# Kernel tuning notes

Hardware: AMD Instinct MI355X
Metric: run time of the kernel (lower is better)

Reference implementation:

```python
import jax, jax.numpy as jnp
import numpy as np

N0, N1, N2, N3 = 100000, 25000, 6250, 1600
DEG = 16
D_IN, D_H = 512, 256


def setup_inputs() -> dict:
    key = jax.random.key(0)
    ks = jax.random.split(key, 20)
    inp = {}
    inp["x"] = jax.random.normal(ks[0], (N0, D_IN), dtype=jnp.float32)
    # bipartite blocks: (src_ids into previous frontier, dst_ids into next frontier)
    inp["src0"] = jax.random.randint(ks[1], (N1 * DEG,), 0, N0)
    inp["dst0"] = jax.random.randint(ks[2], (N1 * DEG,), 0, N1)
    inp["src1"] = jax.random.randint(ks[3], (N2 * DEG,), 0, N1)
    inp["dst1"] = jax.random.randint(ks[4], (N2 * DEG,), 0, N2)
    inp["src2"] = jax.random.randint(ks[5], (N3 * DEG,), 0, N2)
    inp["dst2"] = jax.random.randint(ks[6], (N3 * DEG,), 0, N3)
    def xavier(k, shp):
        fan_in, fan_out = shp
        lim = jnp.sqrt(6.0 / (fan_in + fan_out))
        return jax.random.uniform(k, shp, jnp.float32, -lim, lim)
    inp["Ws0"] = xavier(ks[7], (D_IN, D_H)); inp["Wn0"] = xavier(ks[8], (D_IN, D_H)); inp["b0"] = jnp.zeros((D_H,), jnp.float32)
    inp["Ws1"] = xavier(ks[9], (D_H, D_H)); inp["Wn1"] = xavier(ks[10], (D_H, D_H)); inp["b1"] = jnp.zeros((D_H,), jnp.float32)
    inp["Ws2"] = xavier(ks[11], (D_H, D_H)); inp["Wn2"] = xavier(ks[12], (D_H, D_H)); inp["b2"] = jnp.zeros((D_H,), jnp.float32)
    inp["W_fc"] = xavier(ks[13], (D_H, D_H)); inp["b_fc"] = jnp.zeros((D_H,), jnp.float32)
    return inp


def _sage_mean(h, src, dst, n_dst, Ws, Wn, b):
    # DGL SAGEConv('mean') on a bipartite block: out = h_dst@Ws + mean_neigh@Wn + b
    h_dst = h[:n_dst]                                   # [n_dst, d]
    msg = h[src]                                        # [E, d] gather
    agg = jax.ops.segment_sum(msg, dst, num_segments=n_dst)
    deg = jax.ops.segment_sum(jnp.ones(src.shape, h.dtype), dst, num_segments=n_dst)
    mean = agg / jnp.maximum(deg, 1.0)[:, None]
    return h_dst @ Ws + mean @ Wn + b


def reference(x, src0, dst0, src1, dst1, src2, dst2,
              Ws0, Wn0, b0, Ws1, Wn1, b1, Ws2, Wn2, b2, W_fc, b_fc):
    h = _sage_mean(x, src0, dst0, N1, Ws0, Wn0, b0)
    h = jax.nn.relu(h)  # dropout is identity in eval mode
    h = _sage_mean(h, src1, dst1, N2, Ws1, Wn1, b1)
    h = jax.nn.relu(h)
    h = _sage_mean(h, src2, dst2, N3, Ws2, Wn2, b2)
    return h @ W_fc + b_fc
```

## Files before the change

### kernel.cpp

```cpp
#include <hip/hip_runtime.h>
#include <hip/hip_bf16.h>
#include <cstddef>
#include <cstdint>

#define N0 100000
#define N1 25000
#define N2 6250
#define N3 1600
#define DEG 16
#define D_IN 512
#define D_H 256

#define E0 (N1*DEG)
#define E1 (N2*DEG)
#define E2 (N3*DEG)

typedef _Float16 half_t;
typedef __attribute__((ext_vector_type(8))) _Float16 f16x8;
typedef __attribute__((ext_vector_type(4))) float f32x4;

#define XB 25000
#define WB 2304
#define HB (((E0+E1+E2) + 255) / 256)

__device__ __forceinline__ void gl_lds16(const void* g, void* l)
{
    __builtin_amdgcn_global_load_lds(
        (const __attribute__((address_space(1))) void*)g,
        (__attribute__((address_space(3))) void*)l,
        16, 0, 0);
}

__global__ __launch_bounds__(256)
void mega_conv_kernel(const float* __restrict__ x, half_t* __restrict__ xh,
                      const float* s0, const float* s1, const float* s2, const float* s3,
                      const float* s4, const float* s5, const float* s6,
                      half_t* t0, half_t* t1, half_t* t2, half_t* t3,
                      half_t* t4, half_t* t5, half_t* t6,
                      const int* __restrict__ d0, const int* __restrict__ d1,
                      const int* __restrict__ d2,
                      int* __restrict__ c0, int* __restrict__ c1, int* __restrict__ c2)
{
    const int bid = blockIdx.x;
    if (bid < XB) {
        const int id = bid * 256 + threadIdx.x;
        const float4* p = reinterpret_cast<const float4*>(x) + (size_t)id * 2;
        const float4 a = p[0], b = p[1];
        f16x8 o;
        o[0] = (half_t)a.x; o[1] = (half_t)a.y; o[2] = (half_t)a.z; o[3] = (half_t)a.w;
        o[4] = (half_t)b.x; o[5] = (half_t)b.y; o[6] = (half_t)b.z; o[7] = (half_t)b.w;
        *(reinterpret_cast<f16x8*>(xh) + id) = o;
    } else if (bid < XB + WB) {
        const int id = (bid - XB) * 256 + threadIdx.x;
        const float* src; half_t* dst; int kb; int e;
        if (id < 131072)      { src = s0; dst = t0; kb = 9; e = id; }
        else if (id < 262144) { src = s1; dst = t1; kb = 9; e = id - 131072; }
        else if (id < 327680) { src = s2; dst = t2; kb = 8; e = id - 262144; }
        else if (id < 393216) { src = s3; dst = t3; kb = 8; e = id - 327680; }
        else if (id < 458752) { src = s4; dst = t4; kb = 8; e = id - 393216; }
        else if (id < 524288) { src = s5; dst = t5; kb = 8; e = id - 458752; }
        else if (id < 589824) { src = s6; dst = t6; kb = 8; e = id - 524288; }
        else return;
        const int K = 1 << kb;
        const int nn = e >> kb, k = e & (K - 1);
        dst[((size_t)nn << kb) + k] = (half_t)src[(size_t)k * 256 + nn];
    } else {
        const int i = (bid - XB - WB) * 256 + threadIdx.x;
        if (i < E0)                atomicAdd(&c0[d0[i]], 1);
        else if (i < E0 + E1)      atomicAdd(&c1[d1[i - E0]], 1);
        else if (i < E0 + E1 + E2) atomicAdd(&c2[d2[i - E0 - E1]], 1);
    }
}

__global__ void fill3_kernel(const int* __restrict__ s0, const int* __restrict__ d0,
                             const int* __restrict__ s1, const int* __restrict__ d1,
                             const int* __restrict__ s2, const int* __restrict__ d2,
                             int* __restrict__ u0, int* __restrict__ u1, int* __restrict__ u2,
                             int* __restrict__ e0, int* __restrict__ e1, int* __restrict__ e2)
{
    const int i = blockIdx.x * 256 + threadIdx.x;
    if (i < E0) {
        const int p = atomicAdd(&u0[d0[i]], 1); e0[p] = s0[i];
    } else if (i < E0 + E1) {
        const int j = i - E0;
        const int p = atomicAdd(&u1[d1[j]], 1); e1[p] = s1[j];
    } else if (i < E0 + E1 + E2) {
        const int j = i - E0 - E1;
        const int p = atomicAdd(&u2[d2[j]], 1); e2[p] = s2[j];
    }
}

__global__ __launch_bounds__(1024)
void scan3_kernel(const int* __restrict__ c0, int* __restrict__ p0, int* __restrict__ u0,
                  const int* __restrict__ c1, int* __restrict__ p1, int* __restrict__ u1,
                  const int* __restrict__ c2, int* __restrict__ p2, int* __restrict__ u2)
{
    const int b = blockIdx.x;
    const int* cnt = (b == 0) ? c0 : (b == 1) ? c1 : c2;
    int* ptr = (b == 0) ? p0 : (b == 1) ? p1 : p2;
    int* cur = (b == 0) ? u0 : (b == 1) ? u1 : u2;
    const int n = (b == 0) ? N1 : (b == 1) ? N2 : N3;

    const int t = threadIdx.x;
    const int chunk = (n + 1023) >> 10;
    const int beg = t * chunk;
    const int end = min(n, beg + chunk);

    int sum = 0;
    for (int i = beg; i < end; ++i) sum += cnt[i];

    const int lane = t & 63, wid = t >> 6;
    int inc = sum;
    #pragma unroll
    for (int d = 1; d < 64; d <<= 1) {
        int u = __shfl_up(inc, d, 64);
        if (lane >= d) inc += u;
    }
    __shared__ int wtot[16];
    __shared__ int total_s;
    if (lane == 63) wtot[wid] = inc;
    __syncthreads();
    if (wid == 0) {
        int w = (lane < 16) ? wtot[lane] : 0;
        int ws = w;
        #pragma unroll
        for (int d = 1; d < 16; d <<= 1) {
            int u = __shfl_up(ws, d, 64);
            if (lane >= d) ws += u;
        }
        if (lane < 16) wtot[lane] = ws - w;
        if (lane == 15) total_s = ws;
    }
    __syncthreads();
    int run = (inc - sum) + wtot[wid];
    for (int i = beg; i < end; ++i) {
        ptr[i] = run; cur[i] = run;
        run += cnt[i];
    }
    if (t == 0) ptr[n] = total_s;
}

template<int K>
__global__ __launch_bounds__(256)
void csr_mean_f16(const half_t* __restrict__ h, const int* __restrict__ esrc,
                  const int* __restrict__ ptr, half_t* __restrict__ mean, int n)
{
    constexpr int TPN = K / 8;
    constexpr int NPB = 256 / TPN;
    const int node = blockIdx.x * NPB + threadIdx.x / TPN;
    const int lane = threadIdx.x % TPN;
    if (node >= n) return;
    const int beg = ptr[node], end = ptr[node + 1];
    float acc[8] = {};
    for (int base = beg; base < end; base += TPN) {
        const int rem = end - base;
        const int cnt = (rem < TPN) ? rem : TPN;
        const int myidx = (lane < cnt) ? esrc[base + lane] : 0;
        int j = 0;
        for (; j + 7 < cnt; j += 8) {
            int a[8];
            #pragma unroll
            for (int u = 0; u < 8; ++u) a[u] = __shfl(myidx, j + u, TPN);
            f16x8 v[8];
            #pragma unroll
            for (int u = 0; u < 8; ++u)
                v[u] = *reinterpret_cast<const f16x8*>(h + (size_t)a[u] * K + (size_t)lane * 8);
            #pragma unroll
            for (int u = 0; u < 8; ++u)
                #pragma unroll
                for (int i = 0; i < 8; ++i) acc[i] += (float)v[u][i];
        }
        for (; j < cnt; ++j) {
            const int a0 = __shfl(myidx, j, TPN);
            const f16x8 v0 = *reinterpret_cast<const f16x8*>(h + (size_t)a0 * K + (size_t)lane * 8);
            #pragma unroll
            for (int i = 0; i < 8; ++i) acc[i] += (float)v0[i];
        }
    }
    const float r = 1.0f / fmaxf((float)(end - beg), 1.0f);
    f16x8 o;
    #pragma unroll
    for (int i = 0; i < 8; ++i) o[i] = (half_t)(acc[i] * r);
    *reinterpret_cast<f16x8*>(mean + (size_t)node * K + (size_t)lane * 8) = o;
}

#define GBM 64
#define GBK 64

template<bool HAS_MEAN, bool RELU, bool OUT_F16>
__global__ __launch_bounds__(512)
void mfma_gemm(const half_t* __restrict__ A,
               const half_t* __restrict__ Mn,
               const half_t* __restrict__ WsT,
               const half_t* __restrict__ WnT,
               const float* __restrict__ bias,
               void* __restrict__ Cout,
               int M, int K)
{
    __shared__ half_t sA[GBM * GBK];
    __shared__ half_t sB[256 * GBK];

    const int tid  = threadIdx.x;
    const int wid  = tid >> 6;
    const int lane = tid & 63;
    const int bm   = blockIdx.x * GBM;

    const int lrow = lane & 15;
    const int kg16 = (lane >> 4) << 4;

    f32x4 acc[4][2] = {};

    const int npass = HAS_MEAN ? 2 : 1;
    for (int pass = 0; pass < npass; ++pass) {
        const half_t* __restrict__ Ap = (HAS_MEAN && pass) ? Mn : A;
        const half_t* __restrict__ Wp = (HAS_MEAN && pass) ? WnT : WsT;

        for (int k0 = 0; k0 < K; k0 += GBK) {
            {
                const int Lb  = wid << 10;
                const int L   = Lb + (lane << 4);
                const int row = L >> 7;
                const int c   = (L & 127) ^ ((row & 7) << 4);
                gl_lds16(Ap + (size_t)(bm + row) * K + k0 + (c >> 1), sA + (Lb >> 1));
            }
            #pragma unroll
            for (int i = 0; i < 4; ++i) {
                const int Lb  = ((i << 3) + wid) << 10;
                const int L   = Lb + (lane << 4);
                const int row = L >> 7;
                const int c   = (L & 127) ^ ((row & 7) << 4);
                gl_lds16(Wp + (size_t)row * K + k0 + (c >> 1), sB + (Lb >> 1));
            }
            __syncthreads();

            #pragma unroll
            for (int kk = 0; kk < 2; ++kk) {
                const int cb = (kk << 6) + kg16;
                f16x8 af[4], bf[2];
                #pragma unroll
                for (int m = 0; m < 4; ++m) {
                    const int row = m * 16 + lrow;
                    const int c = cb ^ ((row & 7) << 4);
                    af[m] = *reinterpret_cast<const f16x8*>(&sA[row * GBK + (c >> 1)]);
                }
                #pragma unroll
                for (int n = 0; n < 2; ++n) {
                    const int row = wid * 32 + n * 16 + lrow;
                    const int c = cb ^ ((row & 7) << 4);
                    bf[n] = *reinterpret_cast<const f16x8*>(&sB[row * GBK + (c >> 1)]);
                }
                #pragma unroll
                for (int m = 0; m < 4; ++m)
                    #pragma unroll
                    for (int n = 0; n < 2; ++n)
                        acc[m][n] = __builtin_amdgcn_mfma_f32_16x16x32_f16(af[m], bf[n], acc[m][n], 0, 0, 0);
            }
            __syncthreads();
        }
    }

    const int lcol = lane & 15;
    const int rgrp = lane >> 4;
    #pragma unroll
    for (int m = 0; m < 4; ++m) {
        #pragma unroll
        for (int n = 0; n < 2; ++n) {
            const int col = wid * 32 + n * 16 + lcol;
            const float bv = bias[col];
            #pragma unroll
            for (int r = 0; r < 4; ++r) {
                const int row = bm + m * 16 + rgrp * 4 + r;
                if (row >= M) continue;
                float v = acc[m][n][r] + bv;
                if (RELU) v = fmaxf(v, 0.0f);
                if (OUT_F16) ((half_t*)Cout)[(size_t)row * 256 + col] = (half_t)v;
                else         ((float*)Cout)[(size_t)row * 256 + col] = v;
            }
        }
    }
}

static constexpr size_t align256(size_t x) { return (x + 255) & ~(size_t)255; }

extern "C" void kernel_launch(void* const* d_in, const int* in_sizes, int n_in,
                              void* d_out, int out_size, void* d_ws, size_t ws_size,
                              hipStream_t stream)
{
    const float* x    = (const float*)d_in[0];
    const int*  src0  = (const int*)d_in[1];
    const int*  dst0  = (const int*)d_in[2];
    const int*  src1  = (const int*)d_in[3];
    const int*  dst1  = (const int*)d_in[4];
    const int*  src2  = (const int*)d_in[5];
    const int*  dst2  = (const int*)d_in[6];
    const float* Ws0  = (const float*)d_in[7];
    const float* Wn0  = (const float*)d_in[8];
    const float* b0   = (const float*)d_in[9];
    const float* Ws1  = (const float*)d_in[10];
    const float* Wn1  = (const float*)d_in[11];
    const float* b1   = (const float*)d_in[12];
    const float* Ws2  = (const float*)d_in[13];
    const float* Wn2  = (const float*)d_in[14];
    const float* b2   = (const float*)d_in[15];
    const float* W_fc = (const float*)d_in[16];
    const float* b_fc = (const float*)d_in[17];
    float* out = (float*)d_out;

    char* ws = (char*)d_ws;
    size_t off = 0;
    const size_t cntA_off = off; off = align256(off + (size_t)(N1 + N2 + N3) * 4);
    const size_t ptr0_off = off; off = align256(off + (size_t)(N1 + 1) * 4);
    const size_t ptr1_off = off; off = align256(off + (size_t)(N2 + 1) * 4);
    const size_t ptr2_off = off; off = align256(off + (size_t)(N3 + 1) * 4);
    const size_t cur0_off = off; off = align256(off + (size_t)N1 * 4);
    const size_t cur1_off = off; off = align256(off + (size_t)N2 * 4);
    const size_t cur2_off = off; off = align256(off + (size_t)N3 * 4);
    const size_t es0_off  = off; off = align256(off + (size_t)E0 * 4);
    const size_t es1_off  = off; off = align256(off + (size_t)E1 * 4);
    const size_t es2_off  = off; off = align256(off + (size_t)E2 * 4);
    const size_t xh_off   = off; off = align256(off + (size_t)N0 * D_IN * 2);
    const size_t mean_off = off; off = align256(off + (size_t)N1 * D_IN * 2);
    const size_t h0_off   = off; off = align256(off + (size_t)N1 * D_H * 2);
    const size_t h1_off   = off; off = align256(off + (size_t)N2 * D_H * 2);
    const size_t h2_off   = off; off = align256(off + (size_t)N3 * D_H * 2);
    const size_t wt0_off  = off; off = align256(off + (size_t)D_IN * D_H * 2);
    const size_t wt1_off  = off; off = align256(off + (size_t)D_IN * D_H * 2);
    const size_t wt2_off  = off; off = align256(off + (size_t)D_H * D_H * 2);
    const size_t wt3_off  = off; off = align256(off + (size_t)D_H * D_H * 2);
    const size_t wt4_off  = off; off = align256(off + (size_t)D_H * D_H * 2);
    const size_t wt5_off  = off; off = align256(off + (size_t)D_H * D_H * 2);
    const size_t wt6_off  = off; off = align256(off + (size_t)D_H * D_H * 2);

    int* cnt0 = (int*)(ws + cntA_off);
    int* cnt1 = cnt0 + N1;
    int* cnt2 = cnt1 + N2;
    int* ptr0 = (int*)(ws + ptr0_off);
    int* ptr1 = (int*)(ws + ptr1_off);
    int* ptr2 = (int*)(ws + ptr2_off);
    int* cur0 = (int*)(ws + cur0_off);
    int* cur1 = (int*)(ws + cur1_off);
    int* cur2 = (int*)(ws + cur2_off);
    int* es0  = (int*)(ws + es0_off);
    int* es1  = (int*)(ws + es1_off);
    int* es2  = (int*)(ws + es2_off);
    half_t* xh   = (half_t*)(ws + xh_off);
    half_t* mean = (half_t*)(ws + mean_off);
    half_t* h0   = (half_t*)(ws + h0_off);
    half_t* h1   = (half_t*)(ws + h1_off);
    half_t* h2   = (half_t*)(ws + h2_off);
    half_t* WsT0 = (half_t*)(ws + wt0_off);
    half_t* WnT0 = (half_t*)(ws + wt1_off);
    half_t* WsT1 = (half_t*)(ws + wt2_off);
    half_t* WnT1 = (half_t*)(ws + wt3_off);
    half_t* WsT2 = (half_t*)(ws + wt4_off);
    half_t* WnT2 = (half_t*)(ws + wt5_off);
    half_t* WfcT = (half_t*)(ws + wt6_off);

    hipMemsetAsync(cnt0, 0, (size_t)(N1 + N2 + N3) * 4, stream);
    mega_conv_kernel<<<XB + WB + HB, 256, 0, stream>>>(
        x, xh,
        Ws0, Wn0, Ws1, Wn1, Ws2, Wn2, W_fc,
        WsT0, WnT0, WsT1, WnT1, WsT2, WnT2, WfcT,
        dst0, dst1, dst2, cnt0, cnt1, cnt2);
    scan3_kernel<<<3, 1024, 0, stream>>>(cnt0, ptr0, cur0, cnt1, ptr1, cur1, cnt2, ptr2, cur2);
    {
        const int tot = E0 + E1 + E2;
        fill3_kernel<<<(tot + 255) / 256, 256, 0, stream>>>(
            src0, dst0, src1, dst1, src2, dst2, cur0, cur1, cur2, es0, es1, es2);
    }

    {
        constexpr int NPB = 256 / (D_IN / 8);
        csr_mean_f16<D_IN><<<(N1 + NPB - 1) / NPB, 256, 0, stream>>>(xh, es0, ptr0, mean, N1);
        mfma_gemm<true, true, true><<<(N1 + GBM - 1) / GBM, 512, 0, stream>>>(
            xh, mean, WsT0, WnT0, b0, h0, N1, D_IN);
    }
    {
        constexpr int NPB = 256 / (D_H / 8);
        csr_mean_f16<D_H><<<(N2 + NPB - 1) / NPB, 256, 0, stream>>>(h0, es1, ptr1, mean, N2);
        mfma_gemm<true, true, true><<<(N2 + GBM - 1) / GBM, 512, 0, stream>>>(
            h0, mean, WsT1, WnT1, b1, h1, N2, D_H);
    }
    {
        constexpr int NPB = 256 / (D_H / 8);
        csr_mean_f16<D_H><<<(N3 + NPB - 1) / NPB, 256, 0, stream>>>(h1, es2, ptr2, mean, N3);
        mfma_gemm<true, false, true><<<(N3 + GBM - 1) / GBM, 512, 0, stream>>>(
            h1, mean, WsT2, WnT2, b2, h2, N3, D_H);
    }
    mfma_gemm<false, false, false><<<(N3 + GBM - 1) / GBM, 512, 0, stream>>>(
        h2, nullptr, WfcT, nullptr, b_fc, out, N3, D_H);
}
```

Before: 288.7 us.

## Split x fp16 conversion by column halves and overlap with layer-0 gather

The fp32->fp16 conversion of x is split into two column halves. The low half is converted in the front kernel alongside the weight transposes and degree counting. The high half is converted in a second kernel that interleaves, one block in five, the neighbor-mean gather over the already converted low columns. A final kernel gathers the high columns. The aim is to overlap the bandwidth-heavy conversion with the random-access gather, at the cost of an extra launch and two half-width gather passes that each re-read the edge lists.

After: 291.9 us. No clear change (+1.1%).

```diff
diff --git a/kernel.cpp b/kernel.cpp
--- a/kernel.cpp
+++ b/kernel.cpp
@@ -19,7 +19,7 @@
 typedef __attribute__((ext_vector_type(8))) _Float16 f16x8;
 typedef __attribute__((ext_vector_type(4))) float f32x4;
 
-#define XB 25000
+#define XLB 12500
 #define WB 2304
 #define HB (((E0+E1+E2) + 255) / 256)
 
@@ -31,27 +31,77 @@
         16, 0, 0);
 }
 
+template<int COFF>
+__device__ __forceinline__ void xconv_half(const float* __restrict__ x,
+                                           half_t* __restrict__ xh, int t)
+{
+    const int r = t >> 5;
+    const int c = COFF + ((t & 31) << 3);
+    const float4* p = reinterpret_cast<const float4*>(x + (size_t)r * D_IN + c);
+    const float4 a = p[0], b = p[1];
+    f16x8 o;
+    o[0] = (half_t)a.x; o[1] = (half_t)a.y; o[2] = (half_t)a.z; o[3] = (half_t)a.w;
+    o[4] = (half_t)b.x; o[5] = (half_t)b.y; o[6] = (half_t)b.z; o[7] = (half_t)b.w;
+    *reinterpret_cast<f16x8*>(xh + (size_t)r * D_IN + c) = o;
+}
+
+template<int COFF>
+__device__ __forceinline__ void gather_half_node(
+    const half_t* __restrict__ feat, const int* __restrict__ esrc,
+    const int* __restrict__ ptr, half_t* __restrict__ mean,
+    int node, int gl, int n)
+{
+    constexpr int TPN = 32;
+    if (node >= n) return;
+    const int beg = ptr[node], end = ptr[node + 1];
+    float acc[8] = {};
+    for (int base = beg; base < end; base += TPN) {
+        const int rem = end - base;
+        const int cnt = (rem < TPN) ? rem : TPN;
+        const int myidx = (gl < cnt) ? esrc[base + gl] : 0;
+        int j = 0;
+        for (; j + 7 < cnt; j += 8) {
+            int a[8];
+            #pragma unroll
+            for (int u = 0; u < 8; ++u) a[u] = __shfl(myidx, j + u, TPN);
+            f16x8 v[8];
+            #pragma unroll
+            for (int u = 0; u < 8; ++u)
+                v[u] = *reinterpret_cast<const f16x8*>(feat + (size_t)a[u] * D_IN + COFF + (size_t)gl * 8);
+            #pragma unroll
+            for (int u = 0; u < 8; ++u)
+                #pragma unroll
+                for (int i = 0; i < 8; ++i) acc[i] += (float)v[u][i];
+        }
+        for (; j < cnt; ++j) {
+            const int a0 = __shfl(myidx, j, TPN);
+            const f16x8 v0 = *reinterpret_cast<const f16x8*>(feat + (size_t)a0 * D_IN + COFF + (size_t)gl * 8);
+            #pragma unroll
+            for (int i = 0; i < 8; ++i) acc[i] += (float)v0[i];
+        }
+    }
+    const float r = 1.0f / fmaxf((float)(end - beg), 1.0f);
+    f16x8 o;
+    #pragma unroll
+    for (int i = 0; i < 8; ++i) o[i] = (half_t)(acc[i] * r);
+    *reinterpret_cast<f16x8*>(mean + (size_t)node * D_IN + COFF + (size_t)gl * 8) = o;
+}
+
 __global__ __launch_bounds__(256)
-void mega_conv_kernel(const float* __restrict__ x, half_t* __restrict__ xh,
-                      const float* s0, const float* s1, const float* s2, const float* s3,
-                      const float* s4, const float* s5, const float* s6,
-                      half_t* t0, half_t* t1, half_t* t2, half_t* t3,
-                      half_t* t4, half_t* t5, half_t* t6,
-                      const int* __restrict__ d0, const int* __restrict__ d1,
-                      const int* __restrict__ d2,
-                      int* __restrict__ c0, int* __restrict__ c1, int* __restrict__ c2)
+void front1_kernel(const float* __restrict__ x, half_t* __restrict__ xh,
+                   const float* s0, const float* s1, const float* s2, const float* s3,
+                   const float* s4, const float* s5, const float* s6,
+                   half_t* t0, half_t* t1, half_t* t2, half_t* t3,
+                   half_t* t4, half_t* t5, half_t* t6,
+                   const int* __restrict__ d0, const int* __restrict__ d1,
+                   const int* __restrict__ d2,
+                   int* __restrict__ c0, int* __restrict__ c1, int* __restrict__ c2)
 {
     const int bid = blockIdx.x;
-    if (bid < XB) {
-        const int id = bid * 256 + threadIdx.x;
-        const float4* p = reinterpret_cast<const float4*>(x) + (size_t)id * 2;
-        const float4 a = p[0], b = p[1];
-        f16x8 o;
-        o[0] = (half_t)a.x; o[1] = (half_t)a.y; o[2] = (half_t)a.z; o[3] = (half_t)a.w;
-        o[4] = (half_t)b.x; o[5] = (half_t)b.y; o[6] = (half_t)b.z; o[7] = (half_t)b.w;
-        *(reinterpret_cast<f16x8*>(xh) + id) = o;
-    } else if (bid < XB + WB) {
-        const int id = (bid - XB) * 256 + threadIdx.x;
+    if (bid < XLB) {
+        xconv_half<0>(x, xh, bid * 256 + threadIdx.x);
+    } else if (bid < XLB + WB) {
+        const int id = (bid - XLB) * 256 + threadIdx.x;
         const float* src; half_t* dst; int kb; int e;
         if (id < 131072)      { src = s0; dst = t0; kb = 9; e = id; }
         else if (id < 262144) { src = s1; dst = t1; kb = 9; e = id - 131072; }
@@ -65,11 +115,38 @@
         const int nn = e >> kb, k = e & (K - 1);
         dst[((size_t)nn << kb) + k] = (half_t)src[(size_t)k * 256 + nn];
     } else {
-        const int i = (bid - XB - WB) * 256 + threadIdx.x;
+        const int i = (bid - XLB - WB) * 256 + threadIdx.x;
         if (i < E0)                atomicAdd(&c0[d0[i]], 1);
         else if (i < E0 + E1)      atomicAdd(&c1[d1[i - E0]], 1);
         else if (i < E0 + E1 + E2) atomicAdd(&c2[d2[i - E0 - E1]], 1);
     }
+}
+
+__global__ __launch_bounds__(256)
+void front2_kernel(const float* __restrict__ x, half_t* __restrict__ xh,
+                   const int* __restrict__ esrc, const int* __restrict__ ptr,
+                   half_t* __restrict__ mean)
+{
+    const int bid = blockIdx.x;
+    if ((bid % 5) == 4) {
+        const int g = bid / 5;
+        gather_half_node<0>(xh, esrc, ptr, mean,
+                            g * 8 + (int)(threadIdx.x >> 5),
+                            (int)(threadIdx.x & 31), N1);
+    } else {
+        const int cidx = bid - bid / 5;
+        xconv_half<256>(x, xh, cidx * 256 + threadIdx.x);
+    }
+}
+
+__global__ __launch_bounds__(256)
+void gather_hi_kernel(const half_t* __restrict__ xh,
+                      const int* __restrict__ esrc, const int* __restrict__ ptr,
+                      half_t* __restrict__ mean)
+{
+    gather_half_node<256>(xh, esrc, ptr, mean,
+                          blockIdx.x * 8 + (int)(threadIdx.x >> 5),
+                          (int)(threadIdx.x & 31), N1);
 }
 
 __global__ void fill3_kernel(const int* __restrict__ s0, const int* __restrict__ d0,
@@ -357,7 +434,7 @@
     half_t* WfcT = (half_t*)(ws + wt6_off);
 
     hipMemsetAsync(cnt0, 0, (size_t)(N1 + N2 + N3) * 4, stream);
-    mega_conv_kernel<<<XB + WB + HB, 256, 0, stream>>>(
+    front1_kernel<<<XLB + WB + HB, 256, 0, stream>>>(
         x, xh,
         Ws0, Wn0, Ws1, Wn1, Ws2, Wn2, W_fc,
         WsT0, WnT0, WsT1, WnT1, WsT2, WnT2, WfcT,
@@ -368,13 +445,11 @@
         fill3_kernel<<<(tot + 255) / 256, 256, 0, stream>>>(
             src0, dst0, src1, dst1, src2, dst2, cur0, cur1, cur2, es0, es1, es2);
     }
-
-    {
-        constexpr int NPB = 256 / (D_IN / 8);
-        csr_mean_f16<D_IN><<<(N1 + NPB - 1) / NPB, 256, 0, stream>>>(xh, es0, ptr0, mean, N1);
-        mfma_gemm<true, true, true><<<(N1 + GBM - 1) / GBM, 512, 0, stream>>>(
-            xh, mean, WsT0, WnT0, b0, h0, N1, D_IN);
-    }
+    front2_kernel<<<XLB + 3125, 256, 0, stream>>>(x, xh, es0, ptr0, mean);
+    gather_hi_kernel<<<3125, 256, 0, stream>>>(xh, es0, ptr0, mean);
+
+    mfma_gemm<true, true, true><<<(N1 + GBM - 1) / GBM, 512, 0, stream>>>(
+        xh, mean, WsT0, WnT0, b0, h0, N1, D_IN);
     {
         constexpr int NPB = 256 / (D_H / 8);
         csr_mean_f16<D_H><<<(N2 + NPB - 1) / NPB, 256, 0, stream>>>(h0, es1, ptr1, mean, N2);
```
